# Optimization experiments

Hardware: AMD Instinct MI355X
Metric: run time of the kernel (lower is better)

## Reference

```python
import jax, jax.numpy as jnp
import numpy as np

B, S, H, N, D, R = 2, 2048, 768, 12, 64, 5  # batch, seq, hidden, heads, head_dim, n_structural_deps


def setup_inputs() -> dict:
    key = jax.random.key(0)
    ks = jax.random.split(key, 12)
    hidden_states = jax.random.normal(ks[0], (B, S, H), dtype=jnp.float32)
    attention_mask = jnp.zeros((B, 1, 1, S), dtype=jnp.float32)  # additive mask, all-visible
    # binary structural adjacency per dependency, broadcast over heads
    graph_adj = (jax.random.uniform(ks[1], (R, B, 1, S, S)) < 0.1).astype(jnp.float32)
    s = 0.02
    Wq = jax.random.normal(ks[2], (H, H), dtype=jnp.float32) * s
    bq = jnp.zeros((H,), dtype=jnp.float32)
    Wk = jax.random.normal(ks[3], (H, H), dtype=jnp.float32) * s
    bk = jnp.zeros((H,), dtype=jnp.float32)
    Wv = jax.random.normal(ks[4], (H, H), dtype=jnp.float32) * s
    bv = jnp.zeros((H,), dtype=jnp.float32)
    # biaffine bilinear forms, one [N, D, D] per structural dependency
    bili = jax.random.normal(ks[5], (R, N, D, D), dtype=jnp.float32) * s
    abs_bias = jnp.zeros((R, N), dtype=jnp.float32)  # initialized to zeros as in torch
    return {
        'hidden_states': hidden_states, 'attention_mask': attention_mask,
        'graph_adj': graph_adj, 'Wq': Wq, 'bq': bq, 'Wk': Wk, 'bk': bk,
        'Wv': Wv, 'bv': bv, 'bili': bili, 'abs_bias': abs_bias, 'layer_idx': 0,
    }


def reference(hidden_states, attention_mask, graph_adj, Wq, bq, Wk, bk, Wv, bv,
              bili, abs_bias, layer_idx):
    b, s, h = hidden_states.shape
    n, d = N, D

    def heads(x):  # [b, s, h] -> [b, n, s, d]
        return x.reshape(b, s, n, d).transpose(0, 2, 1, 3)

    q = heads(hidden_states @ Wq.T + bq)
    k = heads(hidden_states @ Wk.T + bk)
    v = heads(hidden_states @ Wv.T + bv)

    scores = jnp.einsum('bnid,bnjd->bnij', q, k)  # [b, n, s, s]
    # biaffine structural bias per dependency, masked by graph adjacency
    for i in range(R):  # small fixed structural loop
        bias = jnp.einsum('bnip,npq,bnjq->bnij', q, bili[i], k)
        bias = bias + abs_bias[i][None, :, None, None]
        scores = scores + bias * graph_adj[i]

    scores = scores / np.sqrt(d).astype(np.float32) + attention_mask
    probs = jax.nn.softmax(scores, axis=-1)
    ctx = jnp.einsum('bnij,bnjd->bnid', probs, v)  # [b, n, s, d]
    return ctx.transpose(0, 2, 1, 3).reshape(b, s, h)
```

## Files before the change

kernel.cpp:

```cpp
#include <hip/hip_runtime.h>
#include <cstdint>
#include <cstddef>

#define B_  2
#define S_  2048
#define H_  768
#define NH  12
#define DH  64
#define RD  5
#define BN  (B_*NH)

typedef _Float16 f16;
typedef __attribute__((ext_vector_type(8))) _Float16 f16x8;
typedef __attribute__((ext_vector_type(4))) float f32x4;

#define MFMA16(a, b, c) __builtin_amdgcn_mfma_f32_16x16x32_f16((a), (b), (c), 0, 0, 0)

#if __has_builtin(__builtin_amdgcn_exp2f)
__device__ __forceinline__ float exp2fast(float x) { return __builtin_amdgcn_exp2f(x); }
#else
__device__ __forceinline__ float exp2fast(float x) { return __expf(0.69314718056f * x); }
#endif

#define SCL 0.1803368801f
#define L2E 1.44269504f

#define NX4 ((B_*S_*H_)/4)
#define NW4 ((H_*H_)/4)

__global__ __launch_bounds__(256) void cvtall(
    const float* __restrict__ x,
    const float* __restrict__ wq, const float* __restrict__ wk,
    const float* __restrict__ wv,
    f16* __restrict__ xh, f16* __restrict__ wh)
{
    int idx = blockIdx.x * 256 + threadIdx.x;
    const int total4 = NX4 + 3 * NW4;
    if (idx >= total4) return;
    const float* src;
    f16* dst;
    int off;
    if (idx < NX4) {
        src = x; dst = xh; off = idx;
    } else {
        int r = idx - NX4;
        int which = r / NW4;
        off = r - which * NW4;
        src = (which == 0) ? wq : (which == 1) ? wk : wv;
        dst = wh + (size_t)which * H_ * H_;
    }
    float4 f = ((const float4*)src)[off];
    f16 h[4] = {(f16)f.x, (f16)f.y, (f16)f.z, (f16)f.w};
    ((ushort4*)dst)[off] = *(const ushort4*)h;
}

__global__ __launch_bounds__(256, 3) void qkv_gemm(
    const f16* __restrict__ xh, const f16* __restrict__ wh,
    const float* __restrict__ bq, const float* __restrict__ bk,
    const float* __restrict__ bv,
    f16* __restrict__ qo, f16* __restrict__ ko, f16* __restrict__ vt)
{
    __shared__ __align__(16) f16 Xs[64][72];
    __shared__ __align__(16) f16 Ws[3][64][72];

    const int tid = threadIdx.x;
    const int n  = blockIdx.x;
    const int m0 = blockIdx.y * 64;
    const int w = tid >> 6, lane = tid & 63;
    const int l15 = lane & 15, quad = lane >> 4;
    const int srow = tid >> 2, sc0 = (tid & 3) * 16;

    f32x4 acc[3][4];
#pragma unroll
    for (int i = 0; i < 3; ++i)
#pragma unroll
        for (int ns = 0; ns < 4; ++ns) acc[i][ns] = (f32x4){0.f, 0.f, 0.f, 0.f};

    const f16* xsrc = xh + (size_t)(m0 + srow) * H_ + sc0;
    const f16* wsrc = wh + (size_t)(n * 64 + srow) * H_ + sc0;

    for (int kc = 0; kc < 12; ++kc) {
        __syncthreads();
        {
            const f16* s0 = xsrc + kc * 64;
            *(f16x8*)&Xs[srow][sc0]     = *(const f16x8*)(s0);
            *(f16x8*)&Xs[srow][sc0 + 8] = *(const f16x8*)(s0 + 8);
        }
#pragma unroll
        for (int i = 0; i < 3; ++i) {
            const f16* s0 = wsrc + (size_t)i * H_ * H_ + kc * 64;
            *(f16x8*)&Ws[i][srow][sc0]     = *(const f16x8*)(s0);
            *(f16x8*)&Ws[i][srow][sc0 + 8] = *(const f16x8*)(s0 + 8);
        }
        __syncthreads();

        f16x8 a0 = *(const f16x8*)&Xs[w * 16 + l15][quad * 8];
        f16x8 a1 = *(const f16x8*)&Xs[w * 16 + l15][quad * 8 + 32];
#pragma unroll
        for (int i = 0; i < 3; ++i)
#pragma unroll
            for (int ns = 0; ns < 4; ++ns) {
                f16x8 b0 = *(const f16x8*)&Ws[i][ns * 16 + l15][quad * 8];
                f16x8 b1 = *(const f16x8*)&Ws[i][ns * 16 + l15][quad * 8 + 32];
                acc[i][ns] = MFMA16(a0, b0, acc[i][ns]);
                acc[i][ns] = MFMA16(a1, b1, acc[i][ns]);
            }
    }
    __syncthreads();

    const float* bias[3] = {bq, bk, bv};
    f16 (*T0)[72] = Xs;
    f16 (*T1)[72] = Ws[0];
    f16 (*T2)[72] = Ws[1];
#pragma unroll
    for (int i = 0; i < 3; ++i) {
        f16 (*T)[72] = (i == 0) ? T0 : (i == 1) ? T1 : T2;
#pragma unroll
        for (int ns = 0; ns < 4; ++ns) {
            float bb = bias[i][n * 64 + ns * 16 + l15];
#pragma unroll
            for (int reg = 0; reg < 4; ++reg)
                T[w * 16 + quad * 4 + reg][ns * 16 + l15] =
                    (f16)(acc[i][ns][reg] + bb);
        }
    }
    __syncthreads();

    const int mrow = m0 + srow;
    const int bb2 = mrow >> 11, ss = mrow & 2047;
    {
        f16* dst = qo + ((size_t)(bb2 * NH + n) * S_ + ss) * DH + sc0;
        *(f16x8*)dst       = *(const f16x8*)&T0[srow][sc0];
        *(f16x8*)(dst + 8) = *(const f16x8*)&T0[srow][sc0 + 8];
    }
    {
        f16* dst = ko + ((size_t)(bb2 * NH + n) * S_ + ss) * DH + sc0;
        *(f16x8*)dst       = *(const f16x8*)&T1[srow][sc0];
        *(f16x8*)(dst + 8) = *(const f16x8*)&T1[srow][sc0 + 8];
    }
    {
        f16 tmp[16];
#pragma unroll
        for (int u = 0; u < 16; ++u) tmp[u] = T2[sc0 + u][srow];
        f16* dst = vt + ((size_t)(bb2 * NH + n) * DH + srow) * S_ + (m0 & 2047) + sc0;
        *(f16x8*)dst       = *(const f16x8*)&tmp[0];
        *(f16x8*)(dst + 8) = *(const f16x8*)&tmp[8];
    }
}

__global__ __launch_bounds__(256) void adjpack(
    const float* __restrict__ adj, unsigned char* __restrict__ adjp)
{
    const int idx4 = blockIdx.x * 256 + threadIdx.x;
    const int j4 = idx4 & 511;
    const int iq = (idx4 >> 9) & 511;
    const int b  = idx4 >> 18;
    unsigned int wbits[4] = {0, 0, 0, 0};
#pragma unroll
    for (int r = 0; r < RD; ++r) {
#pragma unroll
        for (int ii = 0; ii < 4; ++ii) {
            float4 v = *(const float4*)(adj +
                (((size_t)(r * B_ + b) * S_) + iq * 4 + ii) * S_ + j4 * 4);
            float vv[4] = {v.x, v.y, v.z, v.w};
#pragma unroll
            for (int jj = 0; jj < 4; ++jj)
                wbits[jj] |= (vv[jj] != 0.f ? 1u : 0u) << (r + 8 * ii);
        }
    }
    uint4 pk = {wbits[0], wbits[1], wbits[2], wbits[3]};
    *(uint4*)(adjp + ((size_t)(b * 512 + iq) * S_ + j4 * 4) * 4) = pk;
}

__global__ __launch_bounds__(256, 3) void attn(
    const f16* __restrict__ q, const f16* __restrict__ k, const f16* __restrict__ vt,
    const float* __restrict__ bili, const unsigned char* __restrict__ adjp,
    const float* __restrict__ mask, const float* __restrict__ absb,
    float* __restrict__ out)
{
    __shared__ __align__(16) char smem[9216 + 9216 + 128];
    f16*   Mt  = (f16*)smem;
    f16*   Pb  = (f16*)(smem + 9216);
    float* lut = (float*)(smem + 9216 + 9216);

    const int tid = threadIdx.x;
    const int idx = blockIdx.x;
    const int g = idx & 7;
    const int it = (idx >> 3) & 31;
    const int bn = 8 * (idx >> 8) + g;
    const int b = bn / NH, n = bn % NH;
    const int w = tid >> 6, lane = tid & 63;
    const int l15 = lane & 15, quad = lane >> 4;
    const int wi0 = it * 64 + w * 16;
    const size_t kbase = (size_t)bn * S_ * DH;

    if (tid < 32) {
        float a = 0.f;
#pragma unroll
        for (int r = 0; r < RD; ++r)
            if (tid & (1 << r)) a += absb[r * NH + n];
        lut[tid] = a * SCL;
    }

    const f16* qrow = q + kbase + (size_t)(wi0 + l15) * DH + quad * 8;
    f16x8 aq0 = *(const f16x8*)(qrow);
    f16x8 aq1 = *(const f16x8*)(qrow + 32);

    f16* Pw = Pb + w * 16 * 72;

    f16x8 aqp[RD][2];
#pragma unroll 1
    for (int r = 0; r < RD; ++r) {
        __syncthreads();
        {
            int p = tid >> 2, q0 = (tid & 3) * 16;
            const float* src = bili + ((size_t)(r * NH + n) * DH + p) * DH + q0;
            float4 g0 = ((const float4*)src)[0];
            float4 g1 = ((const float4*)src)[1];
            float4 g2 = ((const float4*)src)[2];
            float4 g3 = ((const float4*)src)[3];
            float mv[16] = {g0.x, g0.y, g0.z, g0.w, g1.x, g1.y, g1.z, g1.w,
                            g2.x, g2.y, g2.z, g2.w, g3.x, g3.y, g3.z, g3.w};
#pragma unroll
            for (int u = 0; u < 16; ++u) Mt[(q0 + u) * 72 + p] = (f16)mv[u];
        }
        __syncthreads();
#pragma unroll
        for (int ns = 0; ns < 4; ++ns) {
            f16x8 b0 = *(const f16x8*)&Mt[(ns * 16 + l15) * 72 + quad * 8];
            f16x8 b1 = *(const f16x8*)&Mt[(ns * 16 + l15) * 72 + quad * 8 + 32];
            f32x4 d = {0.f, 0.f, 0.f, 0.f};
            d = MFMA16(aq0, b0, d);
            d = MFMA16(aq1, b1, d);
#pragma unroll
            for (int reg = 0; reg < 4; ++reg)
                Pw[(quad * 4 + reg) * 72 + ns * 16 + l15] = (f16)d[reg];
        }
        aqp[r][0] = *(const f16x8*)&Pw[l15 * 72 + quad * 8];
        aqp[r][1] = *(const f16x8*)&Pw[l15 * 72 + quad * 8 + 32];
    }

    f16x8 ones;
#pragma unroll
    for (int u = 0; u < 8; ++u) ones[u] = (f16)1.0f;

    f32x4 o[4] = {{0,0,0,0},{0,0,0,0},{0,0,0,0},{0,0,0,0}};
    f32x4 lacc = {0.f, 0.f, 0.f, 0.f};
    float mrun[4] = {-1e30f, -1e30f, -1e30f, -1e30f};

    const unsigned char* adjrow =
        adjp + (size_t)(b * 512 + (wi0 >> 2) + quad) * (S_ * 4);
    const float* maskrow = mask + (size_t)b * S_;
    const f16* vtb = vt + (size_t)bn * DH * S_;

    for (int t = 0; t < 32; ++t) {
        const int j0 = t * 64;
        float sc[4][4];

#pragma unroll
        for (int js = 0; js < 4; ++js) {
            const int jcol = j0 + js * 16 + l15;
            const f16* kp = k + kbase + (size_t)jcol * DH + quad * 8;
            f16x8 bk0 = *(const f16x8*)(kp);
            f16x8 bk1 = *(const f16x8*)(kp + 32);

            f32x4 aqk = {0.f, 0.f, 0.f, 0.f};
            aqk = MFMA16(aq0, bk0, aqk);
            aqk = MFMA16(aq1, bk1, aqk);
            f32x4 ar[RD];
#pragma unroll
            for (int r = 0; r < RD; ++r) {
                f32x4 z = {0.f, 0.f, 0.f, 0.f};
                z = MFMA16(aqp[r][0], bk0, z);
                z = MFMA16(aqp[r][1], bk1, z);
                ar[r] = z;
            }

            uchar4 a4 = *(const uchar4*)(adjrow + (size_t)jcol * 4);
            unsigned int bbits[4] = {a4.x, a4.y, a4.z, a4.w};
            float mkL = maskrow[jcol] * L2E;
#pragma unroll
            for (int reg = 0; reg < 4; ++reg) {
                float s = aqk[reg];
                unsigned int bt = bbits[reg];
#pragma unroll
                for (int r = 0; r < RD; ++r)
                    s = fmaf((float)((bt >> r) & 1u), ar[r][reg], s);
                sc[js][reg] = fmaf(s, SCL, lut[bt] + mkL);
            }
        }

        float alpha[4];
#pragma unroll
        for (int reg = 0; reg < 4; ++reg) {
            float nm = fmaxf(fmaxf(sc[0][reg], sc[1][reg]),
                             fmaxf(sc[2][reg], sc[3][reg]));
#pragma unroll
            for (int off = 1; off < 16; off <<= 1)
                nm = fmaxf(nm, __shfl_xor(nm, off));
            float mn = fmaxf(mrun[reg], nm);
            alpha[reg] = exp2fast(mrun[reg] - mn);
            mrun[reg] = mn;
        }
#pragma unroll
        for (int js = 0; js < 4; ++js)
#pragma unroll
            for (int reg = 0; reg < 4; ++reg) {
                float p = exp2fast(sc[js][reg] - mrun[reg]);
                Pw[(quad * 4 + reg) * 72 + js * 16 + l15] = (f16)p;
            }
#pragma unroll
        for (int reg = 0; reg < 4; ++reg) {
            lacc[reg] *= alpha[reg];
#pragma unroll
            for (int ds = 0; ds < 4; ++ds) o[ds][reg] *= alpha[reg];
        }

        f16x8 pa0 = *(const f16x8*)&Pw[l15 * 72 + quad * 8];
        f16x8 pa1 = *(const f16x8*)&Pw[l15 * 72 + quad * 8 + 32];
        lacc = MFMA16(pa0, ones, lacc);
        lacc = MFMA16(pa1, ones, lacc);
#pragma unroll
        for (int ds = 0; ds < 4; ++ds) {
            const f16* vp = vtb + (size_t)(ds * 16 + l15) * S_ + j0 + quad * 8;
            f16x8 bv0 = *(const f16x8*)(vp);
            f16x8 bv1 = *(const f16x8*)(vp + 32);
            o[ds] = MFMA16(pa0, bv0, o[ds]);
            o[ds] = MFMA16(pa1, bv1, o[ds]);
        }
    }

#pragma unroll
    for (int reg = 0; reg < 4; ++reg) {
        float inv = 1.f / lacc[reg];
        int i = wi0 + quad * 4 + reg;
#pragma unroll
        for (int ds = 0; ds < 4; ++ds)
            out[((size_t)b * S_ + i) * H_ + n * DH + ds * 16 + l15] =
                o[ds][reg] * inv;
    }
}

extern "C" void kernel_launch(void* const* d_in, const int* in_sizes, int n_in,
                              void* d_out, int out_size, void* d_ws, size_t ws_size,
                              hipStream_t stream)
{
    const float* hs   = (const float*)d_in[0];
    const float* mask = (const float*)d_in[1];
    const float* adj  = (const float*)d_in[2];
    const float* Wq   = (const float*)d_in[3];
    const float* bq   = (const float*)d_in[4];
    const float* Wk   = (const float*)d_in[5];
    const float* bk   = (const float*)d_in[6];
    const float* Wv   = (const float*)d_in[7];
    const float* bv   = (const float*)d_in[8];
    const float* bili = (const float*)d_in[9];
    const float* absb = (const float*)d_in[10];
    float* out = (float*)d_out;

    const size_t QKV = (size_t)BN * S_ * DH;
    f16* q  = (f16*)d_ws;
    f16* k  = q + QKV;
    f16* vt = k + QKV;
    unsigned char* adjp = (unsigned char*)(vt + QKV);
    f16* xh = (f16*)(adjp + (size_t)B_ * 512 * S_ * 4);
    f16* wh = xh + (size_t)B_ * S_ * H_;

    const int total4 = NX4 + 3 * NW4;
    cvtall<<<(total4 + 255) / 256, 256, 0, stream>>>(hs, Wq, Wk, Wv, xh, wh);
    qkv_gemm<<<dim3(12, 64), 256, 0, stream>>>(xh, wh, bq, bk, bv, q, k, vt);
    adjpack<<<2048, 256, 0, stream>>>(adj, adjp);
    attn<<<768, 256, 0, stream>>>(q, k, vt, bili, adjp, mask, absb, out);
}
```

Before: 517.2 us.

## Split attention key range across two wave groups and merge softmax partials

After: 994.4 us. 1.92x slower.

```diff
diff --git a/kernel.cpp b/kernel.cpp
--- a/kernel.cpp
+++ b/kernel.cpp
@@ -172,16 +172,16 @@
     *(uint4*)(adjp + ((size_t)(b * 512 + iq) * S_ + j4 * 4) * 4) = pk;
 }
 
-__global__ __launch_bounds__(256, 3) void attn(
+__global__ __launch_bounds__(512, 6) void attn(
     const f16* __restrict__ q, const f16* __restrict__ k, const f16* __restrict__ vt,
     const float* __restrict__ bili, const unsigned char* __restrict__ adjp,
     const float* __restrict__ mask, const float* __restrict__ absb,
     float* __restrict__ out)
 {
-    __shared__ __align__(16) char smem[9216 + 9216 + 128];
+    __shared__ __align__(16) char smem[9216 + 18432 + 128];
     f16*   Mt  = (f16*)smem;
     f16*   Pb  = (f16*)(smem + 9216);
-    float* lut = (float*)(smem + 9216 + 9216);
+    float* lut = (float*)(smem + 9216 + 18432);
 
     const int tid = threadIdx.x;
     const int idx = blockIdx.x;
@@ -190,8 +190,10 @@
     const int bn = 8 * (idx >> 8) + g;
     const int b = bn / NH, n = bn % NH;
     const int w = tid >> 6, lane = tid & 63;
+    const int half = w >> 2;
+    const int wq = w & 3;
     const int l15 = lane & 15, quad = lane >> 4;
-    const int wi0 = it * 64 + w * 16;
+    const int wi0 = it * 64 + wq * 16;
     const size_t kbase = (size_t)bn * S_ * DH;
 
     if (tid < 32) {
@@ -212,7 +214,7 @@
 #pragma unroll 1
     for (int r = 0; r < RD; ++r) {
         __syncthreads();
-        {
+        if (tid < 256) {
             int p = tid >> 2, q0 = (tid & 3) * 16;
             const float* src = bili + ((size_t)(r * NH + n) * DH + p) * DH + q0;
             float4 g0 = ((const float4*)src)[0];
@@ -253,7 +255,8 @@
     const float* maskrow = mask + (size_t)b * S_;
     const f16* vtb = vt + (size_t)bn * DH * S_;
 
-    for (int t = 0; t < 32; ++t) {
+    const int t0 = half * 16;
+    for (int t = t0; t < t0 + 16; ++t) {
         const int j0 = t * 64;
         float sc[4][4];
 
@@ -330,14 +333,37 @@
         }
     }
 
-#pragma unroll
-    for (int reg = 0; reg < 4; ++reg) {
-        float inv = 1.f / lacc[reg];
-        int i = wi0 + quad * 4 + reg;
+    __syncthreads();
+    float* ex = (float*)smem;
+    if (half) {
+        float* p = ex + ((size_t)(wq * 64 + lane)) * 25;
 #pragma unroll
         for (int ds = 0; ds < 4; ++ds)
-            out[((size_t)b * S_ + i) * H_ + n * DH + ds * 16 + l15] =
-                o[ds][reg] * inv;
+#pragma unroll
+            for (int reg = 0; reg < 4; ++reg) p[ds * 4 + reg] = o[ds][reg];
+#pragma unroll
+        for (int reg = 0; reg < 4; ++reg) {
+            p[16 + reg] = lacc[reg];
+            p[20 + reg] = mrun[reg];
+        }
+    }
+    __syncthreads();
+    if (!half) {
+        const float* p = ex + ((size_t)(wq * 64 + lane)) * 25;
+#pragma unroll
+        for (int reg = 0; reg < 4; ++reg) {
+            float m2 = p[20 + reg];
+            float mN = fmaxf(mrun[reg], m2);
+            float c1 = exp2fast(mrun[reg] - mN);
+            float c2 = exp2fast(m2 - mN);
+            float l  = lacc[reg] * c1 + p[16 + reg] * c2;
+            float inv = 1.f / l;
+            int i = wi0 + quad * 4 + reg;
+#pragma unroll
+            for (int ds = 0; ds < 4; ++ds)
+                out[((size_t)b * S_ + i) * H_ + n * DH + ds * 16 + l15] =
+                    (o[ds][reg] * c1 + p[ds * 4 + reg] * c2) * inv;
+        }
     }
 }
 
@@ -370,5 +396,5 @@
     cvtall<<<(total4 + 255) / 256, 256, 0, stream>>>(hs, Wq, Wk, Wv, xh, wh);
     qkv_gemm<<<dim3(12, 64), 256, 0, stream>>>(xh, wh, bq, bk, bv, q, k, vt);
     adjpack<<<2048, 256, 0, stream>>>(adj, adjp);
-    attn<<<768, 256, 0, stream>>>(q, k, vt, bili, adjp, mask, absb, out);
+    attn<<<768, 512, 0, stream>>>(q, k, vt, bili, adjp, mask, absb, out);
 }
```

## Split attention KV range in two and merge partial softmax results

Applied to the files above, without the earlier changes.

Result: slower. 564.0 us (+9.1%).

```diff
diff --git a/kernel.cpp b/kernel.cpp
--- a/kernel.cpp
+++ b/kernel.cpp
@@ -176,7 +176,7 @@
     const f16* __restrict__ q, const f16* __restrict__ k, const f16* __restrict__ vt,
     const float* __restrict__ bili, const unsigned char* __restrict__ adjp,
     const float* __restrict__ mask, const float* __restrict__ absb,
-    float* __restrict__ out)
+    float* __restrict__ po, float* __restrict__ pm, float* __restrict__ pl)
 {
     __shared__ __align__(16) char smem[9216 + 9216 + 128];
     f16*   Mt  = (f16*)smem;
@@ -187,7 +187,8 @@
     const int idx = blockIdx.x;
     const int g = idx & 7;
     const int it = (idx >> 3) & 31;
-    const int bn = 8 * (idx >> 8) + g;
+    const int half = (idx >> 8) & 1;
+    const int bn = 8 * (idx >> 9) + g;
     const int b = bn / NH, n = bn % NH;
     const int w = tid >> 6, lane = tid & 63;
     const int l15 = lane & 15, quad = lane >> 4;
@@ -253,7 +254,8 @@
     const float* maskrow = mask + (size_t)b * S_;
     const f16* vtb = vt + (size_t)bn * DH * S_;
 
-    for (int t = 0; t < 32; ++t) {
+    const int t0 = half * 16;
+    for (int t = t0; t < t0 + 16; ++t) {
         const int j0 = t * 64;
         float sc[4][4];
 
@@ -330,15 +332,45 @@
         }
     }
 
+    const size_t rbase = (size_t)(half * BN + bn) * S_;
 #pragma unroll
     for (int reg = 0; reg < 4; ++reg) {
-        float inv = 1.f / lacc[reg];
         int i = wi0 + quad * 4 + reg;
+        float* prow = po + (rbase + i) * 64;
 #pragma unroll
         for (int ds = 0; ds < 4; ++ds)
-            out[((size_t)b * S_ + i) * H_ + n * DH + ds * 16 + l15] =
-                o[ds][reg] * inv;
-    }
+            prow[ds * 16 + l15] = o[ds][reg];
+        if (l15 == 0) {
+            pm[rbase + i] = mrun[reg];
+            pl[rbase + i] = lacc[reg];
+        }
+    }
+}
+
+__global__ __launch_bounds__(256) void merge(
+    const float* __restrict__ po, const float* __restrict__ pm,
+    const float* __restrict__ pl, float* __restrict__ out)
+{
+    const int t = blockIdx.x * 256 + threadIdx.x;
+    const int rid = t >> 4;
+    const int d4 = t & 15;
+    const int bn = rid >> 11, row = rid & 2047;
+    const int b = bn / NH, n = bn % NH;
+
+    const float m0 = pm[rid], m1 = pm[BN * S_ + rid];
+    const float l0 = pl[rid], l1 = pl[BN * S_ + rid];
+    const float mN = fmaxf(m0, m1);
+    const float c0 = exp2fast(m0 - mN), c1 = exp2fast(m1 - mN);
+    const float inv = 1.f / (l0 * c0 + l1 * c1);
+
+    const float4 o0 = ((const float4*)po)[(size_t)rid * 16 + d4];
+    const float4 o1 = ((const float4*)po)[((size_t)BN * S_ + rid) * 16 + d4];
+    float4 r;
+    r.x = (o0.x * c0 + o1.x * c1) * inv;
+    r.y = (o0.y * c0 + o1.y * c1) * inv;
+    r.z = (o0.z * c0 + o1.z * c1) * inv;
+    r.w = (o0.w * c0 + o1.w * c1) * inv;
+    ((float4*)out)[(size_t)(b * S_ + row) * (H_ / 4) + n * (DH / 4) + d4] = r;
 }
 
 extern "C" void kernel_launch(void* const* d_in, const int* in_sizes, int n_in,
@@ -365,10 +397,14 @@
     unsigned char* adjp = (unsigned char*)(vt + QKV);
     f16* xh = (f16*)(adjp + (size_t)B_ * 512 * S_ * 4);
     f16* wh = xh + (size_t)B_ * S_ * H_;
+    float* po = (float*)(wh + (size_t)3 * H_ * H_);
+    float* pm = po + (size_t)2 * BN * S_ * DH;
+    float* pl = pm + (size_t)2 * BN * S_;
 
     const int total4 = NX4 + 3 * NW4;
     cvtall<<<(total4 + 255) / 256, 256, 0, stream>>>(hs, Wq, Wk, Wv, xh, wh);
     qkv_gemm<<<dim3(12, 64), 256, 0, stream>>>(xh, wh, bq, bk, bv, q, k, vt);
     adjpack<<<2048, 256, 0, stream>>>(adj, adjp);
-    attn<<<768, 256, 0, stream>>>(q, k, vt, bili, adjp, mask, absb, out);
-}
+    attn<<<1536, 256, 0, stream>>>(q, k, vt, bili, adjp, mask, absb, po, pm, pl);
+    merge<<<3072, 256, 0, stream>>>(po, pm, pl, out);
+}
```

## Software-pipeline score computation with softmax/PV across key tiles

Applied to the files above, without the earlier changes.

After: 922.7 us. +78.4%, slower.

```diff
diff --git a/kernel.cpp b/kernel.cpp
--- a/kernel.cpp
+++ b/kernel.cpp
@@ -209,7 +209,7 @@
     f16* Pw = Pb + w * 16 * 72;
 
     f16x8 aqp[RD][2];
-#pragma unroll 1
+#pragma unroll
     for (int r = 0; r < RD; ++r) {
         __syncthreads();
         {
@@ -253,82 +253,91 @@
     const float* maskrow = mask + (size_t)b * S_;
     const f16* vtb = vt + (size_t)bn * DH * S_;
 
-    for (int t = 0; t < 32; ++t) {
-        const int j0 = t * 64;
-        float sc[4][4];
-
-#pragma unroll
-        for (int js = 0; js < 4; ++js) {
-            const int jcol = j0 + js * 16 + l15;
-            const f16* kp = k + kbase + (size_t)jcol * DH + quad * 8;
-            f16x8 bk0 = *(const f16x8*)(kp);
-            f16x8 bk1 = *(const f16x8*)(kp + 32);
-
-            f32x4 aqk = {0.f, 0.f, 0.f, 0.f};
-            aqk = MFMA16(aq0, bk0, aqk);
-            aqk = MFMA16(aq1, bk1, aqk);
-            f32x4 ar[RD];
-#pragma unroll
-            for (int r = 0; r < RD; ++r) {
-                f32x4 z = {0.f, 0.f, 0.f, 0.f};
-                z = MFMA16(aqp[r][0], bk0, z);
-                z = MFMA16(aqp[r][1], bk1, z);
-                ar[r] = z;
-            }
-
-            uchar4 a4 = *(const uchar4*)(adjrow + (size_t)jcol * 4);
-            unsigned int bbits[4] = {a4.x, a4.y, a4.z, a4.w};
-            float mkL = maskrow[jcol] * L2E;
-#pragma unroll
-            for (int reg = 0; reg < 4; ++reg) {
-                float s = aqk[reg];
-                unsigned int bt = bbits[reg];
-#pragma unroll
-                for (int r = 0; r < RD; ++r)
-                    s = fmaf((float)((bt >> r) & 1u), ar[r][reg], s);
-                sc[js][reg] = fmaf(s, SCL, lut[bt] + mkL);
-            }
-        }
-
-        float alpha[4];
-#pragma unroll
-        for (int reg = 0; reg < 4; ++reg) {
-            float nm = fmaxf(fmaxf(sc[0][reg], sc[1][reg]),
-                             fmaxf(sc[2][reg], sc[3][reg]));
-#pragma unroll
-            for (int off = 1; off < 16; off <<= 1)
-                nm = fmaxf(nm, __shfl_xor(nm, off));
-            float mn = fmaxf(mrun[reg], nm);
-            alpha[reg] = exp2fast(mrun[reg] - mn);
-            mrun[reg] = mn;
-        }
-#pragma unroll
-        for (int js = 0; js < 4; ++js)
-#pragma unroll
-            for (int reg = 0; reg < 4; ++reg) {
-                float p = exp2fast(sc[js][reg] - mrun[reg]);
-                Pw[(quad * 4 + reg) * 72 + js * 16 + l15] = (f16)p;
-            }
-#pragma unroll
-        for (int reg = 0; reg < 4; ++reg) {
-            lacc[reg] *= alpha[reg];
-#pragma unroll
-            for (int ds = 0; ds < 4; ++ds) o[ds][reg] *= alpha[reg];
-        }
-
-        f16x8 pa0 = *(const f16x8*)&Pw[l15 * 72 + quad * 8];
-        f16x8 pa1 = *(const f16x8*)&Pw[l15 * 72 + quad * 8 + 32];
-        lacc = MFMA16(pa0, ones, lacc);
-        lacc = MFMA16(pa1, ones, lacc);
-#pragma unroll
-        for (int ds = 0; ds < 4; ++ds) {
-            const f16* vp = vtb + (size_t)(ds * 16 + l15) * S_ + j0 + quad * 8;
-            f16x8 bv0 = *(const f16x8*)(vp);
-            f16x8 bv1 = *(const f16x8*)(vp + 32);
-            o[ds] = MFMA16(pa0, bv0, o[ds]);
-            o[ds] = MFMA16(pa1, bv1, o[ds]);
-        }
-    }
+#define SCORES(T, SC) do {                                                   \
+    const int j0_ = (T) * 64;                                                \
+    _Pragma("unroll")                                                        \
+    for (int js = 0; js < 4; ++js) {                                         \
+        const int jcol = j0_ + js * 16 + l15;                                \
+        const f16* kp = k + kbase + (size_t)jcol * DH + quad * 8;            \
+        f16x8 bk0 = *(const f16x8*)(kp);                                     \
+        f16x8 bk1 = *(const f16x8*)(kp + 32);                                \
+        f32x4 aqk = {0.f, 0.f, 0.f, 0.f};                                    \
+        aqk = MFMA16(aq0, bk0, aqk);                                         \
+        aqk = MFMA16(aq1, bk1, aqk);                                         \
+        uchar4 a4 = *(const uchar4*)(adjrow + (size_t)jcol * 4);             \
+        unsigned int c0 = a4.x, c1 = a4.y, c2 = a4.z, c3 = a4.w;             \
+        float mkL = maskrow[jcol] * L2E;                                     \
+        float s0 = aqk[0], s1 = aqk[1], s2 = aqk[2], s3 = aqk[3];            \
+        _Pragma("unroll")                                                    \
+        for (int r = 0; r < RD; ++r) {                                       \
+            f32x4 z = {0.f, 0.f, 0.f, 0.f};                                  \
+            z = MFMA16(aqp[r][0], bk0, z);                                   \
+            z = MFMA16(aqp[r][1], bk1, z);                                   \
+            s0 = fmaf((float)((c0 >> r) & 1u), z[0], s0);                    \
+            s1 = fmaf((float)((c1 >> r) & 1u), z[1], s1);                    \
+            s2 = fmaf((float)((c2 >> r) & 1u), z[2], s2);                    \
+            s3 = fmaf((float)((c3 >> r) & 1u), z[3], s3);                    \
+        }                                                                    \
+        SC[js][0] = fmaf(s0, SCL, lut[c0] + mkL);                            \
+        SC[js][1] = fmaf(s1, SCL, lut[c1] + mkL);                            \
+        SC[js][2] = fmaf(s2, SCL, lut[c2] + mkL);                            \
+        SC[js][3] = fmaf(s3, SCL, lut[c3] + mkL);                            \
+    }                                                                        \
+} while (0)
+
+#define SMPV(T, SC) do {                                                     \
+    const int j0_ = (T) * 64;                                                \
+    float alpha[4];                                                          \
+    _Pragma("unroll")                                                        \
+    for (int reg = 0; reg < 4; ++reg) {                                      \
+        float nm = fmaxf(fmaxf(SC[0][reg], SC[1][reg]),                      \
+                         fmaxf(SC[2][reg], SC[3][reg]));                     \
+        _Pragma("unroll")                                                    \
+        for (int off = 1; off < 16; off <<= 1)                               \
+            nm = fmaxf(nm, __shfl_xor(nm, off));                             \
+        float mn = fmaxf(mrun[reg], nm);                                     \
+        alpha[reg] = exp2fast(mrun[reg] - mn);                               \
+        mrun[reg] = mn;                                                      \
+    }                                                                        \
+    _Pragma("unroll")                                                        \
+    for (int js = 0; js < 4; ++js)                                           \
+        _Pragma("unroll")                                                    \
+        for (int reg = 0; reg < 4; ++reg) {                                  \
+            float p = exp2fast(SC[js][reg] - mrun[reg]);                     \
+            Pw[(quad * 4 + reg) * 72 + js * 16 + l15] = (f16)p;              \
+        }                                                                    \
+    _Pragma("unroll")                                                        \
+    for (int reg = 0; reg < 4; ++reg) {                                      \
+        lacc[reg] *= alpha[reg];                                             \
+        _Pragma("unroll")                                                    \
+        for (int ds = 0; ds < 4; ++ds) o[ds][reg] *= alpha[reg];             \
+    }                                                                        \
+    f16x8 pa0 = *(const f16x8*)&Pw[l15 * 72 + quad * 8];                     \
+    f16x8 pa1 = *(const f16x8*)&Pw[l15 * 72 + quad * 8 + 32];                 \
+    lacc = MFMA16(pa0, ones, lacc);                                          \
+    lacc = MFMA16(pa1, ones, lacc);                                          \
+    _Pragma("unroll")                                                        \
+    for (int ds = 0; ds < 4; ++ds) {                                         \
+        const f16* vp = vtb + (size_t)(ds * 16 + l15) * S_ + j0_ + quad * 8; \
+        f16x8 bv0 = *(const f16x8*)(vp);                                     \
+        f16x8 bv1 = *(const f16x8*)(vp + 32);                                \
+        o[ds] = MFMA16(pa0, bv0, o[ds]);                                     \
+        o[ds] = MFMA16(pa1, bv1, o[ds]);                                     \
+    }                                                                        \
+} while (0)
+
+    float scA[4][4], scB[4][4];
+    SCORES(0, scA);
+#pragma unroll 1
+    for (int tt = 0; tt < 16; ++tt) {
+        SCORES(2 * tt + 1, scB);
+        SMPV(2 * tt, scA);
+        if (tt < 15) SCORES(2 * tt + 2, scA);
+        SMPV(2 * tt + 1, scB);
+    }
+
+#undef SCORES
+#undef SMPV
 
 #pragma unroll
     for (int reg = 0; reg < 4; ++reg) {
```
